# Performance work log

Hardware: AMD Instinct MI355X
Metric: run time of the kernel (lower is better)

The kernel has to match this reference:

```python
import jax, jax.numpy as jnp
import numpy as np

N, D, K = 65536, 64, 64


def setup_inputs() -> dict:
    key = jax.random.key(0)
    k1, k2, k3, k4, k5 = jax.random.split(key, 5)
    # seed z = (u, x): u ~ U[0,1), x ~ N(0, I_d)
    u = jax.random.uniform(k1, (N, 1), dtype=jnp.float32)
    x = jax.random.normal(k2, (N, D), dtype=jnp.float32)
    z = jnp.concatenate([u, x], axis=-1)  # [N, d+1]
    # parameters, sized/initialized as in GaussianMixture.__init__
    means = 3.0 * jax.random.normal(k3, (K, D), dtype=jnp.float32)
    devsqrt = jnp.eye(D, dtype=jnp.float32) + 0.3 * jax.random.normal(k4, (K, D, D), dtype=jnp.float32)
    devs = jnp.einsum('kij,klj->kil', devsqrt, devsqrt)  # devsqrt @ devsqrt.T per mode
    mix = jax.nn.softmax(jax.random.normal(k5, (K,), dtype=jnp.float32))
    mix_partition = jnp.cumsum(mix)  # [K], monotone boundaries in (0, 1]
    return {"z": z, "means": means, "devs": devs, "mix_partition": mix_partition}


def reference(z, means, devs, mix_partition):
    # split z -> (u, x)
    u = z[..., 0]          # [N]
    x = z[..., 1:]         # [N, d]
    k = means.shape[0]
    # torch.bucketize(u, partition, right=True) == searchsorted side='right'
    idx = jnp.searchsorted(mix_partition, u, side='right')
    idx = jnp.clip(idx, 0, k - 1)  # guard u == 1.0 edge case
    # y = means[i] + devs[i] @ x  (gather fused with batched matvec)
    dy = jnp.einsum('nij,nj->ni', devs[idx], x)
    return means[idx] + dy
```

## Files before the change

### kernel.cpp

```cpp
#include <hip/hip_runtime.h>
#include <hip/hip_bf16.h>
#include <stdint.h>

#define NROWS 65536
#define KMIX 64
#define DD 64
#define ZS 65
#define CHUNK 128
#define PADN (NROWS + KMIX * CHUNK)
#define NBLK4 (PADN / CHUNK)

typedef __bf16 bf16x8 __attribute__((ext_vector_type(8)));
typedef float f32x4 __attribute__((ext_vector_type(4)));

__device__ __forceinline__ unsigned short f2bf(float f) {
  unsigned int x = __float_as_uint(f);
  unsigned int r = (x + 0x7FFFu + ((x >> 16) & 1u)) >> 16;
  return (unsigned short)r;
}

__device__ __forceinline__ void scan_offsets(const uint32_t* __restrict__ counts,
                                             uint32_t* __restrict__ s_off, int t) {
  uint32_t c = counts[t];
  uint32_t p = ((c + CHUNK - 1) / CHUNK) * CHUNK;
  uint32_t inc = p;
  #pragma unroll
  for (int d = 1; d < 64; d <<= 1) {
    uint32_t v = __shfl_up(inc, d, 64);
    if (t >= d) inc += v;
  }
  s_off[t] = inc - p;
  if (t == 63) s_off[64] = inc;
}

__global__ __launch_bounds__(256) void k_idx(
    const float* __restrict__ z, const float* __restrict__ mix,
    uint32_t* __restrict__ idx_arr, uint32_t* __restrict__ counts) {
  __shared__ float s_mix[KMIX];
  __shared__ uint32_t s_hist[KMIX];
  int t = threadIdx.x;
  if (t < KMIX) { s_mix[t] = mix[t]; s_hist[t] = 0u; }
  __syncthreads();
  int n = blockIdx.x * 256 + t;
  float u = z[n * ZS];
  int idx = 0;
  #pragma unroll
  for (int k = 0; k < KMIX; ++k) idx += (s_mix[k] <= u) ? 1 : 0;
  if (idx > KMIX - 1) idx = KMIX - 1;
  idx_arr[n] = (uint32_t)idx;
  atomicAdd(&s_hist[idx], 1u);
  __syncthreads();
  if (t < KMIX && s_hist[t]) atomicAdd(&counts[t], s_hist[t]);
}

__global__ __launch_bounds__(256) void k_scatter(
    const uint32_t* __restrict__ idx_arr, const uint32_t* __restrict__ counts,
    uint32_t* __restrict__ cursors, uint32_t* __restrict__ sorted) {
  __shared__ uint32_t s_off[KMIX + 1];
  __shared__ uint32_t h[KMIX];
  __shared__ uint32_t base[KMIX];
  int t = threadIdx.x;
  if (t < KMIX) { h[t] = 0u; scan_offsets(counts, s_off, t); }
  __syncthreads();
  int n = blockIdx.x * 256 + t;
  uint32_t k = idx_arr[n];
  uint32_t r = atomicAdd(&h[k], 1u);
  __syncthreads();
  if (t < KMIX) base[t] = s_off[t] + (h[t] ? atomicAdd(&cursors[t], h[t]) : 0u);
  __syncthreads();
  sorted[base[k] + r] = (uint32_t)n;
}

__global__ __launch_bounds__(512) void k_main(
    const float* __restrict__ z, const float* __restrict__ means,
    const float* __restrict__ devs, const uint32_t* __restrict__ sorted,
    const uint32_t* __restrict__ counts, float* __restrict__ out) {
  __shared__ uint32_t s_off[KMIX + 1];
  __shared__ uint32_t s_ent[CHUNK];
  __shared__ __align__(16) unsigned short s_devs[DD * 72];
  __shared__ __align__(16) unsigned short s_x[CHUNK * 72];

  const int t = threadIdx.x;
  const int base = blockIdx.x * CHUNK;
  const int lane = t & 63, wave = t >> 6;

  if (t < KMIX) scan_offsets(counts, s_off, t);
  __syncthreads();

  int kb = 0;
  while (kb < KMIX - 1 && s_off[kb + 1] <= (uint32_t)base) ++kb;
  int nv = (int)counts[kb] - (base - (int)s_off[kb]);
  if (nv <= 0) return;
  if (nv > CHUNK) nv = CHUNK;

  if (t < CHUNK) s_ent[t] = (t < nv) ? sorted[base + t] : 0u;

  {
    const float4* gd = reinterpret_cast<const float4*>(devs + (size_t)kb * DD * DD);
    #pragma unroll
    for (int it = 0; it < 2; ++it) {
      int e = t + it * 512;
      float4 v = gd[e];
      int row = e >> 4, col = (e & 15) * 4;
      ushort4 w = make_ushort4(f2bf(v.x), f2bf(v.y), f2bf(v.z), f2bf(v.w));
      *reinterpret_cast<ushort4*>(&s_devs[row * 72 + col]) = w;
    }
  }
  {
    #pragma unroll
    for (int rr = 0; rr < CHUNK; rr += 8) {
      int rl = rr + wave;
      uint32_t row = (rl < nv) ? sorted[base + rl] : sorted[base];
      float xv = z[(size_t)row * ZS + 1 + lane];
      s_x[rl * 72 + lane] = f2bf(xv);
    }
  }
  __syncthreads();

  const int m16 = lane & 15, quad = lane >> 4;

  float mv[4];
  #pragma unroll
  for (int it = 0; it < 4; ++it) mv[it] = means[kb * DD + it * 16 + m16];

  {
    const int g = wave;
    const unsigned short* xr = &s_x[(g * 16 + m16) * 72 + quad * 8];
    bf16x8 a0 = *reinterpret_cast<const bf16x8*>(xr);
    bf16x8 a1 = *reinterpret_cast<const bf16x8*>(xr + 32);

    f32x4 acc[4];
    #pragma unroll
    for (int it = 0; it < 4; ++it) acc[it] = (f32x4){0.f, 0.f, 0.f, 0.f};

    #pragma unroll
    for (int it = 0; it < 4; ++it) {
      const unsigned short* dr = &s_devs[(it * 16 + m16) * 72 + quad * 8];
      bf16x8 b0 = *reinterpret_cast<const bf16x8*>(dr);
      bf16x8 b1 = *reinterpret_cast<const bf16x8*>(dr + 32);
      acc[it] = __builtin_amdgcn_mfma_f32_16x16x32_bf16(a0, b0, acc[it], 0, 0, 0);
      acc[it] = __builtin_amdgcn_mfma_f32_16x16x32_bf16(a1, b1, acc[it], 0, 0, 0);
    }

    #pragma unroll
    for (int reg = 0; reg < 4; ++reg) {
      int rp = g * 16 + quad * 4 + reg;
      if (rp < nv) {
        uint32_t row = s_ent[rp];
        float* orow = out + (size_t)row * DD + m16;
        #pragma unroll
        for (int it = 0; it < 4; ++it) orow[it * 16] = acc[it][reg] + mv[it];
      }
    }
  }
}

extern "C" void kernel_launch(void* const* d_in, const int* in_sizes, int n_in,
                              void* d_out, int out_size, void* d_ws, size_t ws_size,
                              hipStream_t stream) {
  const float* z     = (const float*)d_in[0];
  const float* means = (const float*)d_in[1];
  const float* devs  = (const float*)d_in[2];
  const float* mix   = (const float*)d_in[3];
  float* out = (float*)d_out;

  uint32_t* W = (uint32_t*)d_ws;
  uint32_t* counts  = W;
  uint32_t* cursors = counts + KMIX;
  uint32_t* idx_arr = cursors + KMIX;
  uint32_t* sorted  = idx_arr + NROWS;

  hipMemsetAsync(W, 0, 2 * KMIX * sizeof(uint32_t), stream);

  k_idx<<<NROWS / 256, 256, 0, stream>>>(z, mix, idx_arr, counts);
  k_scatter<<<NROWS / 256, 256, 0, stream>>>(idx_arr, counts, cursors, sorted);
  k_main<<<NBLK4, 512, 0, stream>>>(z, means, devs, sorted, counts, out);
}
```

Measured before the change: 92.83 us.

## Fuse memset, index and scatter into one cooperative kernel with grid syncs

New measurement: 140.9 us. 1.52x slower.

```diff
diff --git a/kernel.cpp b/kernel.cpp
--- a/kernel.cpp
+++ b/kernel.cpp
@@ -1,6 +1,9 @@
 #include <hip/hip_runtime.h>
 #include <hip/hip_bf16.h>
+#include <hip/hip_cooperative_groups.h>
 #include <stdint.h>
+
+namespace cg = cooperative_groups;
 
 #define NROWS 65536
 #define KMIX 64
@@ -33,42 +36,39 @@
   if (t == 63) s_off[64] = inc;
 }
 
-__global__ __launch_bounds__(256) void k_idx(
+__global__ __launch_bounds__(256) void k_sort(
     const float* __restrict__ z, const float* __restrict__ mix,
-    uint32_t* __restrict__ idx_arr, uint32_t* __restrict__ counts) {
+    uint32_t* __restrict__ counts, uint32_t* __restrict__ cursors,
+    uint32_t* __restrict__ sorted) {
+  cg::grid_group grid = cg::this_grid();
   __shared__ float s_mix[KMIX];
   __shared__ uint32_t s_hist[KMIX];
-  int t = threadIdx.x;
+  __shared__ uint32_t s_off[KMIX + 1];
+  __shared__ uint32_t s_base[KMIX];
+
+  const int t = threadIdx.x;
+  const int b = blockIdx.x;
+
+  if (b == 0 && t < 2 * KMIX) ((uint32_t*)counts)[t] = 0u;
   if (t < KMIX) { s_mix[t] = mix[t]; s_hist[t] = 0u; }
-  __syncthreads();
-  int n = blockIdx.x * 256 + t;
-  float u = z[n * ZS];
+  grid.sync();
+
+  const int n = b * 256 + t;
+  float u = z[(size_t)n * ZS];
   int idx = 0;
   #pragma unroll
   for (int k = 0; k < KMIX; ++k) idx += (s_mix[k] <= u) ? 1 : 0;
   if (idx > KMIX - 1) idx = KMIX - 1;
-  idx_arr[n] = (uint32_t)idx;
-  atomicAdd(&s_hist[idx], 1u);
+  uint32_t r = atomicAdd(&s_hist[idx], 1u);
   __syncthreads();
   if (t < KMIX && s_hist[t]) atomicAdd(&counts[t], s_hist[t]);
-}
+  grid.sync();
 
-__global__ __launch_bounds__(256) void k_scatter(
-    const uint32_t* __restrict__ idx_arr, const uint32_t* __restrict__ counts,
-    uint32_t* __restrict__ cursors, uint32_t* __restrict__ sorted) {
-  __shared__ uint32_t s_off[KMIX + 1];
-  __shared__ uint32_t h[KMIX];
-  __shared__ uint32_t base[KMIX];
-  int t = threadIdx.x;
-  if (t < KMIX) { h[t] = 0u; scan_offsets(counts, s_off, t); }
+  if (t < KMIX) scan_offsets(counts, s_off, t);
   __syncthreads();
-  int n = blockIdx.x * 256 + t;
-  uint32_t k = idx_arr[n];
-  uint32_t r = atomicAdd(&h[k], 1u);
+  if (t < KMIX) s_base[t] = s_off[t] + (s_hist[t] ? atomicAdd(&cursors[t], s_hist[t]) : 0u);
   __syncthreads();
-  if (t < KMIX) base[t] = s_off[t] + (h[t] ? atomicAdd(&cursors[t], h[t]) : 0u);
-  __syncthreads();
-  sorted[base[k] + r] = (uint32_t)n;
+  sorted[s_base[idx] + r] = (uint32_t)n;
 }
 
 __global__ __launch_bounds__(512) void k_main(
@@ -167,12 +167,9 @@
   uint32_t* W = (uint32_t*)d_ws;
   uint32_t* counts  = W;
   uint32_t* cursors = counts + KMIX;
-  uint32_t* idx_arr = cursors + KMIX;
-  uint32_t* sorted  = idx_arr + NROWS;
+  uint32_t* sorted  = cursors + KMIX;
 
-  hipMemsetAsync(W, 0, 2 * KMIX * sizeof(uint32_t), stream);
-
-  k_idx<<<NROWS / 256, 256, 0, stream>>>(z, mix, idx_arr, counts);
-  k_scatter<<<NROWS / 256, 256, 0, stream>>>(idx_arr, counts, cursors, sorted);
+  void* args[] = {(void*)&z, (void*)&mix, (void*)&counts, (void*)&cursors, (void*)&sorted};
+  hipLaunchCooperativeKernel((void*)k_sort, dim3(NROWS / 256), dim3(256), args, 0, stream);
   k_main<<<NBLK4, 512, 0, stream>>>(z, means, devs, sorted, counts, out);
 }
```
